# Kernel tuning notes

Measured on AMD Instinct MI355X. Metric: run time of the kernel, lower is better.

The kernel has to match this reference:

```python
import jax, jax.numpy as jnp
import numpy as np

H, V, S = 1024, 50257, 2048

def setup_inputs() -> dict:
    key = jax.random.key(0)
    ks = jax.random.split(key, 13)
    s = 0.02
    return {
        "last_output_word": jax.random.randint(ks[0], (1,), 0, V),
        "last_hidden": jax.random.normal(ks[1], (1, 1, H), dtype=jnp.float32),
        "encoder_outputs": jax.random.normal(ks[2], (S, 1, H), dtype=jnp.float32),
        "embedding": jax.random.normal(ks[3], (V, H), dtype=jnp.float32) * s,
        "attn_W": jax.random.normal(ks[4], (H, 2 * H), dtype=jnp.float32) * s,
        "attn_b": jnp.zeros((H,), dtype=jnp.float32),
        "other": jax.random.normal(ks[5], (1, H), dtype=jnp.float32) * s,
        "W_ih": jax.random.normal(ks[6], (3 * H, 2 * H), dtype=jnp.float32) * s,
        "W_hh": jax.random.normal(ks[7], (3 * H, H), dtype=jnp.float32) * s,
        "b_ih": jnp.zeros((3 * H,), dtype=jnp.float32),
        "b_hh": jnp.zeros((3 * H,), dtype=jnp.float32),
        "out_W": jax.random.normal(ks[8], (V, 2 * H), dtype=jnp.float32) * s,
        "out_b": jnp.zeros((V,), dtype=jnp.float32),
    }

def reference(last_output_word, last_hidden, encoder_outputs, embedding,
              attn_W, attn_b, other, W_ih, W_hh, b_ih, b_hh, out_W, out_b):
    h = last_hidden[-1, 0]                      # [H] top-layer hidden
    enc = encoder_outputs[:, 0, :]              # [S, H]
    # -- concat attention (vectorized over seq_len; no tanh, matches source) --
    cat = jnp.concatenate([jnp.broadcast_to(h[None, :], enc.shape), enc], axis=-1)  # [S, 2H]
    energy = cat @ attn_W.T + attn_b            # [S, H]
    scores = energy @ other[0]                  # [S]
    attn = jax.nn.softmax(scores)               # [S]
    context = attn @ enc                        # [H]
    # -- embedding (dropout = identity in eval) --
    emb = embedding[last_output_word[0]]        # [H]
    # -- single GRU step (torch gate order: r, z, n) --
    x = jnp.concatenate([emb, context])         # [2H]
    gx = W_ih @ x + b_ih                        # [3H]
    gh = W_hh @ h + b_hh                        # [3H]
    r = jax.nn.sigmoid(gx[:H] + gh[:H])
    z = jax.nn.sigmoid(gx[H:2 * H] + gh[H:2 * H])
    n = jnp.tanh(gx[2 * H:] + r * gh[2 * H:])
    h_new = (1.0 - z) * n + z * h               # [H]
    # -- output projection + log-softmax --
    logits = out_W @ jnp.concatenate([h_new, context]) + out_b   # [V]
    log_probs = jax.nn.log_softmax(logits)[None, :]              # [1, V]
    hidden = h_new[None, None, :]                                # [1, 1, H]
    attn_weights = attn[None, None, :]                           # [1, 1, S]
    return (log_probs, hidden, attn_weights)
```

## Files before the change

kernel.cpp:

```cpp
#include <hip/hip_runtime.h>
#include <math.h>

#define HD 1024
#define VD 50257
#define SD 2048


__device__ __forceinline__ float wred(float x) {
#pragma unroll
    for (int o = 32; o; o >>= 1) x += __shfl_down(x, o, 64);
    return x;
}

__global__ __launch_bounds__(256) void k_prep(
        const float* __restrict__ attn_W, const float* __restrict__ other,
        const float* __restrict__ W_hh, const float* __restrict__ h,
        const float* __restrict__ b_hh,
        const float* __restrict__ W_ih, const float* __restrict__ b_ih,
        const float* __restrict__ embedding, const int* __restrict__ word,
        float* __restrict__ ws) {
    float* u2 = ws;
    float* gA = ws + 4096;
    float* gh = ws + 7168;
    const int b = blockIdx.x, t = threadIdx.x;
    if (b < 64) {
        const int ktile = b & 3, jc = b >> 2;
        const int k = ktile * 256 + t;
        const float* Wcol = attn_W + 1024 + k;
        const int j0 = jc * 64;
        float acc = 0.f;
#pragma unroll 4
        for (int j = 0; j < 64; ++j)
            acc += other[j0 + j] * Wcol[(size_t)(j0 + j) * 2048];
        atomicAdd(&u2[k], acc);
    } else if (b < 64 + 768) {
        const int row = (b - 64) * 4 + (t >> 6);
        const int lane = t & 63;
        const float4* p = (const float4*)(W_hh + (size_t)row * 1024);
        const float4* q = (const float4*)h;
        float acc = 0.f;
#pragma unroll
        for (int i = lane; i < 256; i += 64) {
            float4 a = p[i], c = q[i];
            acc += a.x * c.x + a.y * c.y + a.z * c.z + a.w * c.w;
        }
        acc = wred(acc);
        if (lane == 0) gh[row] = acc + b_hh[row];
    } else {
        const int row = (b - 832) * 4 + (t >> 6);
        const int lane = t & 63;
        const float* emb = embedding + (size_t)word[0] * 1024;
        const float4* p = (const float4*)(W_ih + (size_t)row * 2048);
        const float4* q = (const float4*)emb;
        float acc = 0.f;
#pragma unroll
        for (int i = lane; i < 256; i += 64) {
            float4 a = p[i], c = q[i];
            acc += a.x * c.x + a.y * c.y + a.z * c.z + a.w * c.w;
        }
        acc = wred(acc);
        if (lane == 0) gA[row] = acc + b_ih[row];
    }
}

__global__ __launch_bounds__(256) void k_scores(
        const float* __restrict__ enc, const float* __restrict__ ws,
        float* __restrict__ scores) {
    const int row = blockIdx.x * 4 + (threadIdx.x >> 6);
    const int lane = threadIdx.x & 63;
    const float4* p = (const float4*)(enc + (size_t)row * 1024);
    const float4* q = (const float4*)ws;
    float acc = 0.f;
#pragma unroll
    for (int i = lane; i < 256; i += 64) {
        float4 a = p[i], c = q[i];
        acc += a.x * c.x + a.y * c.y + a.z * c.z + a.w * c.w;
    }
    acc = wred(acc);
    if (lane == 0) scores[row] = acc;
}

__global__ __launch_bounds__(256) void k_softmax(
        const float* __restrict__ scores, float* __restrict__ dout) {
    __shared__ float sm[SD];
    __shared__ float wr[8];
    __shared__ float bc;
    const int t = threadIdx.x, lane = t & 63, wave = t >> 6;
    float lm = -INFINITY;
    for (int i = t; i < SD; i += 256) {
        float x = scores[i];
        sm[i] = x;
        lm = fmaxf(lm, x);
    }
#pragma unroll
    for (int o = 32; o; o >>= 1) lm = fmaxf(lm, __shfl_down(lm, o, 64));
    if (lane == 0) wr[wave] = lm;
    __syncthreads();
    if (t == 0) bc = fmaxf(fmaxf(wr[0], wr[1]), fmaxf(wr[2], wr[3]));
    __syncthreads();
    const float M = bc;
    float ls = 0.f;
    for (int i = t; i < SD; i += 256) ls += __expf(sm[i] - M);
#pragma unroll
    for (int o = 32; o; o >>= 1) ls += __shfl_down(ls, o, 64);
    if (lane == 0) wr[4 + wave] = ls;
    __syncthreads();
    if (t == 0) bc = wr[4] + wr[5] + wr[6] + wr[7];
    __syncthreads();
    const float inv = 1.f / bc;
    for (int i = t; i < SD; i += 256) dout[VD + HD + i] = __expf(sm[i] - M) * inv;
}

__global__ __launch_bounds__(256) void k_context(
        const float* __restrict__ enc, const float* __restrict__ dout,
        float* __restrict__ context) {
    const int b = blockIdx.x;
    const int ct = b & 3, rc = b >> 2;
    const int j = ct * 256 + threadIdx.x;
    const float* attn = dout + VD + HD;
    const int r0 = rc * 128;
    float acc = 0.f;
    for (int r = 0; r < 128; ++r)
        acc += attn[r0 + r] * enc[(size_t)(r0 + r) * 1024 + j];
    atomicAdd(&context[j], acc);
}

__global__ __launch_bounds__(256) void k_gru(
        const float* __restrict__ W_ih, const float* __restrict__ h,
        float* __restrict__ ws, float* __restrict__ dout) {
    float* context = ws + 1024;
    float* gA = ws + 4096;
    float* gh = ws + 7168;
    float* y = ws + 10240;
    const int i = blockIdx.x * 4 + (threadIdx.x >> 6);
    const int lane = threadIdx.x & 63;
    const float4* q = (const float4*)context;
    float d[3];
#pragma unroll
    for (int g = 0; g < 3; ++g) {
        const float4* p = (const float4*)(W_ih + (size_t)(g * 1024 + i) * 2048 + 1024);
        float a = 0.f;
#pragma unroll
        for (int k = lane; k < 256; k += 64) {
            float4 x = p[k], c = q[k];
            a += x.x * c.x + x.y * c.y + x.z * c.z + x.w * c.w;
        }
        d[g] = wred(a);
    }
    if (lane == 0) {
        const float r = 1.f / (1.f + __expf(-(gA[i] + d[0] + gh[i])));
        const float z = 1.f / (1.f + __expf(-(gA[1024 + i] + d[1] + gh[1024 + i])));
        const float n = tanhf(gA[2048 + i] + d[2] + r * gh[2048 + i]);
        const float hn = (1.f - z) * n + z * h[i];
        dout[VD + i] = hn;
        y[i] = hn;
        y[1024 + i] = context[i];
    }
}

__global__ __launch_bounds__(256) void k_logits(
        const float* __restrict__ out_W, const float* __restrict__ out_b,
        const float* __restrict__ ws, float* __restrict__ dout) {
    __shared__ float4 sy[512];
    const float4* y4 = (const float4*)(ws + 10240);
    const int t = threadIdx.x;
    sy[t] = y4[t];
    sy[t + 256] = y4[t + 256];
    __syncthreads();
    const int row = blockIdx.x * 4 + (t >> 6);
    if (row >= VD) return;
    const int lane = t & 63;
    const float4* p = (const float4*)(out_W + (size_t)row * 2048);
    float acc = 0.f;
#pragma unroll
    for (int i = lane; i < 512; i += 64) {
        float4 a = p[i];
        float4 b = sy[i];
        acc += a.x * b.x + a.y * b.y + a.z * b.z + a.w * b.w;
    }
    acc = wred(acc);
    if (lane == 0) dout[row] = acc + out_b[row];
}

__global__ __launch_bounds__(256) void k_lse1(
        const float* __restrict__ dout, float* __restrict__ part) {
    __shared__ float wm[4], wsum[4];
    const int t = threadIdx.x, b = blockIdx.x;
    const int lane = t & 63, wave = t >> 6;
    float m = -INFINITY, s = 0.f;
    for (int v = b * 256 + t; v < VD; v += 64 * 256) {
        float x = dout[v];
        float M = fmaxf(m, x);
        s = s * __expf(m - M) + __expf(x - M);
        m = M;
    }
#pragma unroll
    for (int o = 32; o; o >>= 1) {
        float m2 = __shfl_down(m, o, 64), s2 = __shfl_down(s, o, 64);
        float M = fmaxf(m, m2);
        s = s * __expf(m - M) + s2 * __expf(m2 - M);
        m = M;
    }
    if (lane == 0) { wm[wave] = m; wsum[wave] = s; }
    __syncthreads();
    if (t == 0) {
        float M = wm[0], Ss = wsum[0];
#pragma unroll
        for (int w = 1; w < 4; ++w) {
            float M2 = fmaxf(M, wm[w]);
            Ss = Ss * __expf(M - M2) + wsum[w] * __expf(wm[w] - M2);
            M = M2;
        }
        part[2 * b] = M;
        part[2 * b + 1] = Ss;
    }
}

__global__ __launch_bounds__(256) void k_finish(
        float* __restrict__ dout, const float* __restrict__ part) {
    float m = part[0], s = part[1];
#pragma unroll 8
    for (int i = 1; i < 64; ++i) {
        float m2 = part[2 * i], s2 = part[2 * i + 1];
        float M = fmaxf(m, m2);
        s = s * __expf(m - M) + s2 * __expf(m2 - M);
        m = M;
    }
    const float lse = m + logf(s);
    for (int v = blockIdx.x * 256 + threadIdx.x; v < VD; v += gridDim.x * 256)
        dout[v] -= lse;
}

extern "C" void kernel_launch(void* const* d_in, const int* in_sizes, int n_in,
                              void* d_out, int out_size, void* d_ws, size_t ws_size,
                              hipStream_t stream) {
    const int* word = (const int*)d_in[0];
    const float* h = (const float*)d_in[1];
    const float* enc = (const float*)d_in[2];
    const float* embedding = (const float*)d_in[3];
    const float* attn_W = (const float*)d_in[4];
    const float* other = (const float*)d_in[6];
    const float* W_ih = (const float*)d_in[7];
    const float* W_hh = (const float*)d_in[8];
    const float* b_ih = (const float*)d_in[9];
    const float* b_hh = (const float*)d_in[10];
    const float* out_W = (const float*)d_in[11];
    const float* out_b = (const float*)d_in[12];
    float* out = (float*)d_out;
    float* ws = (float*)d_ws;

    hipMemsetAsync(ws, 0, 2048 * sizeof(float), stream);

    k_prep<<<1600, 256, 0, stream>>>(attn_W, other, W_hh, h, b_hh, W_ih, b_ih,
                                     embedding, word, ws);
    k_scores<<<512, 256, 0, stream>>>(enc, ws, ws + 2048);
    k_softmax<<<1, 256, 0, stream>>>(ws + 2048, out);
    k_context<<<64, 256, 0, stream>>>(enc, out, ws + 1024);
    k_gru<<<256, 256, 0, stream>>>(W_ih, h, ws, out);
    k_logits<<<(VD + 3) / 4, 256, 0, stream>>>(out_W, out_b, ws, out);
    k_lse1<<<64, 256, 0, stream>>>(out, ws + 12288);
    k_finish<<<128, 256, 0, stream>>>(out, ws + 12288);
}
```

Measured before the change: 690.8 us.

## Split output projection to overlap context half with GRU and fuse LSE partials

The output projection is split into a context half and an h_new half. The context half runs in the same launch as a fused GRU kernel (input, context and hidden matvecs together), so it no longer waits for the GRU result. Softmax is fused into the context kernel, with each block recomputing it, and the context reduction is spread over more blocks. The h_new-half kernel writes per-block max and sum-of-exp partials, and a final kernel reduces them and subtracts the log-sum-exp. This cuts launches and serialization, at the cost of redundant softmax work and a large partial-reduction repeated in every block of the last kernel.

```diff
diff --git a/kernel.cpp b/kernel.cpp
--- a/kernel.cpp
+++ b/kernel.cpp
@@ -4,6 +4,7 @@
 #define HD 1024
 #define VD 50257
 #define SD 2048
+#define NVB 12565
 
 
 __device__ __forceinline__ float wred(float x) {
@@ -12,55 +13,19 @@
     return x;
 }
 
-__global__ __launch_bounds__(256) void k_prep(
+__global__ __launch_bounds__(256) void k_u2(
         const float* __restrict__ attn_W, const float* __restrict__ other,
-        const float* __restrict__ W_hh, const float* __restrict__ h,
-        const float* __restrict__ b_hh,
-        const float* __restrict__ W_ih, const float* __restrict__ b_ih,
-        const float* __restrict__ embedding, const int* __restrict__ word,
         float* __restrict__ ws) {
-    float* u2 = ws;
-    float* gA = ws + 4096;
-    float* gh = ws + 7168;
     const int b = blockIdx.x, t = threadIdx.x;
-    if (b < 64) {
-        const int ktile = b & 3, jc = b >> 2;
-        const int k = ktile * 256 + t;
-        const float* Wcol = attn_W + 1024 + k;
-        const int j0 = jc * 64;
-        float acc = 0.f;
-#pragma unroll 4
-        for (int j = 0; j < 64; ++j)
-            acc += other[j0 + j] * Wcol[(size_t)(j0 + j) * 2048];
-        atomicAdd(&u2[k], acc);
-    } else if (b < 64 + 768) {
-        const int row = (b - 64) * 4 + (t >> 6);
-        const int lane = t & 63;
-        const float4* p = (const float4*)(W_hh + (size_t)row * 1024);
-        const float4* q = (const float4*)h;
-        float acc = 0.f;
-#pragma unroll
-        for (int i = lane; i < 256; i += 64) {
-            float4 a = p[i], c = q[i];
-            acc += a.x * c.x + a.y * c.y + a.z * c.z + a.w * c.w;
-        }
-        acc = wred(acc);
-        if (lane == 0) gh[row] = acc + b_hh[row];
-    } else {
-        const int row = (b - 832) * 4 + (t >> 6);
-        const int lane = t & 63;
-        const float* emb = embedding + (size_t)word[0] * 1024;
-        const float4* p = (const float4*)(W_ih + (size_t)row * 2048);
-        const float4* q = (const float4*)emb;
-        float acc = 0.f;
-#pragma unroll
-        for (int i = lane; i < 256; i += 64) {
-            float4 a = p[i], c = q[i];
-            acc += a.x * c.x + a.y * c.y + a.z * c.z + a.w * c.w;
-        }
-        acc = wred(acc);
-        if (lane == 0) gA[row] = acc + b_ih[row];
-    }
+    const int kt = b & 3, jc = b >> 2;
+    const int k = kt * 256 + t;
+    const float* Wcol = attn_W + HD + k;
+    const int j0 = jc * 16;
+    float acc = 0.f;
+#pragma unroll
+    for (int j = 0; j < 16; ++j)
+        acc += other[j0 + j] * Wcol[(size_t)(j0 + j) * (2 * HD)];
+    atomicAdd(&ws[k], acc);
 }
 
 __global__ __launch_bounds__(256) void k_scores(
@@ -68,7 +33,7 @@
         float* __restrict__ scores) {
     const int row = blockIdx.x * 4 + (threadIdx.x >> 6);
     const int lane = threadIdx.x & 63;
-    const float4* p = (const float4*)(enc + (size_t)row * 1024);
+    const float4* p = (const float4*)(enc + (size_t)row * HD);
     const float4* q = (const float4*)ws;
     float acc = 0.f;
 #pragma unroll
@@ -80,8 +45,9 @@
     if (lane == 0) scores[row] = acc;
 }
 
-__global__ __launch_bounds__(256) void k_softmax(
-        const float* __restrict__ scores, float* __restrict__ dout) {
+__global__ __launch_bounds__(256) void k_ctx(
+        const float* __restrict__ enc, const float* __restrict__ scores,
+        float* __restrict__ context, float* __restrict__ dout) {
     __shared__ float sm[SD];
     __shared__ float wr[8];
     __shared__ float bc;
@@ -108,90 +74,124 @@
     if (t == 0) bc = wr[4] + wr[5] + wr[6] + wr[7];
     __syncthreads();
     const float inv = 1.f / bc;
-    for (int i = t; i < SD; i += 256) dout[VD + HD + i] = __expf(sm[i] - M) * inv;
-}
-
-__global__ __launch_bounds__(256) void k_context(
-        const float* __restrict__ enc, const float* __restrict__ dout,
-        float* __restrict__ context) {
-    const int b = blockIdx.x;
-    const int ct = b & 3, rc = b >> 2;
-    const int j = ct * 256 + threadIdx.x;
-    const float* attn = dout + VD + HD;
-    const int r0 = rc * 128;
+    for (int i = t; i < SD; i += 256) sm[i] = __expf(sm[i] - M) * inv;
+    __syncthreads();
+    if (blockIdx.x == 0)
+        for (int i = t; i < SD; i += 256) dout[VD + HD + i] = sm[i];
+    const int rc = blockIdx.x >> 2, ct = blockIdx.x & 3;
+    const int j = ct * 256 + t;
+    const int r0 = rc * 64;
     float acc = 0.f;
-    for (int r = 0; r < 128; ++r)
-        acc += attn[r0 + r] * enc[(size_t)(r0 + r) * 1024 + j];
+#pragma unroll 4
+    for (int r = 0; r < 64; ++r)
+        acc += sm[r0 + r] * enc[(size_t)(r0 + r) * HD + j];
     atomicAdd(&context[j], acc);
 }
 
-__global__ __launch_bounds__(256) void k_gru(
-        const float* __restrict__ W_ih, const float* __restrict__ h,
+__global__ __launch_bounds__(256) void k_big(
+        const float* __restrict__ out_W, const float* __restrict__ W_ih,
+        const float* __restrict__ W_hh, const float* __restrict__ b_ih,
+        const float* __restrict__ b_hh, const float* __restrict__ embedding,
+        const int* __restrict__ word, const float* __restrict__ h,
         float* __restrict__ ws, float* __restrict__ dout) {
-    float* context = ws + 1024;
-    float* gA = ws + 4096;
-    float* gh = ws + 7168;
-    float* y = ws + 10240;
-    const int i = blockIdx.x * 4 + (threadIdx.x >> 6);
-    const int lane = threadIdx.x & 63;
-    const float4* q = (const float4*)context;
-    float d[3];
-#pragma unroll
-    for (int g = 0; g < 3; ++g) {
-        const float4* p = (const float4*)(W_ih + (size_t)(g * 1024 + i) * 2048 + 1024);
-        float a = 0.f;
-#pragma unroll
-        for (int k = lane; k < 256; k += 64) {
-            float4 x = p[k], c = q[k];
-            a += x.x * c.x + x.y * c.y + x.z * c.z + x.w * c.w;
-        }
-        d[g] = wred(a);
-    }
-    if (lane == 0) {
-        const float r = 1.f / (1.f + __expf(-(gA[i] + d[0] + gh[i])));
-        const float z = 1.f / (1.f + __expf(-(gA[1024 + i] + d[1] + gh[1024 + i])));
-        const float n = tanhf(gA[2048 + i] + d[2] + r * gh[2048 + i]);
-        const float hn = (1.f - z) * n + z * h[i];
-        dout[VD + i] = hn;
-        y[i] = hn;
-        y[1024 + i] = context[i];
-    }
-}
-
-__global__ __launch_bounds__(256) void k_logits(
+    __shared__ float4 sv[256];
+    const int t = threadIdx.x, lane = t & 63, wave = t >> 6;
+    const float* ctx = ws + 1024;
+    if (blockIdx.x < 256) {
+        const int i = blockIdx.x * 4 + wave;
+        const float4* e4 = (const float4*)(embedding + (size_t)word[0] * HD);
+        const float4* h4 = (const float4*)h;
+        const float4* c4 = (const float4*)ctx;
+        float ga[3], gx[3], gh[3];
+#pragma unroll
+        for (int g = 0; g < 3; ++g) {
+            const int row = g * HD + i;
+            const float4* pa = (const float4*)(W_ih + (size_t)row * 2 * HD);
+            const float4* px = pa + 256;
+            const float4* ph = (const float4*)(W_hh + (size_t)row * HD);
+            float a = 0.f, x = 0.f, hh = 0.f;
+#pragma unroll
+            for (int k = lane; k < 256; k += 64) {
+                float4 w1 = pa[k], w2 = px[k], w3 = ph[k];
+                float4 v1 = e4[k], v2 = c4[k], v3 = h4[k];
+                a += w1.x * v1.x + w1.y * v1.y + w1.z * v1.z + w1.w * v1.w;
+                x += w2.x * v2.x + w2.y * v2.y + w2.z * v2.z + w2.w * v2.w;
+                hh += w3.x * v3.x + w3.y * v3.y + w3.z * v3.z + w3.w * v3.w;
+            }
+            ga[g] = wred(a); gx[g] = wred(x); gh[g] = wred(hh);
+        }
+        if (lane == 0) {
+            const float r = 1.f / (1.f + __expf(-(ga[0] + gx[0] + b_ih[i] + gh[0] + b_hh[i])));
+            const float z = 1.f / (1.f + __expf(-(ga[1] + gx[1] + b_ih[HD + i] + gh[1] + b_hh[HD + i])));
+            const float n = tanhf(ga[2] + gx[2] + b_ih[2 * HD + i] + r * (gh[2] + b_hh[2 * HD + i]));
+            const float hn = (1.f - z) * n + z * h[i];
+            dout[VD + i] = hn;
+            ws[4096 + i] = hn;
+        }
+    } else {
+        sv[t] = ((const float4*)ctx)[t];
+        __syncthreads();
+        const int row = (blockIdx.x - 256) * 4 + wave;
+        if (row >= VD) return;
+        const float4* p = (const float4*)(out_W + (size_t)row * 2 * HD + HD);
+        float acc = 0.f;
+#pragma unroll
+        for (int i = lane; i < 256; i += 64) {
+            float4 a = p[i], c = sv[i];
+            acc += a.x * c.x + a.y * c.y + a.z * c.z + a.w * c.w;
+        }
+        acc = wred(acc);
+        if (lane == 0) ws[8192 + row] = acc;
+    }
+}
+
+__global__ __launch_bounds__(256) void k_fin(
         const float* __restrict__ out_W, const float* __restrict__ out_b,
-        const float* __restrict__ ws, float* __restrict__ dout) {
-    __shared__ float4 sy[512];
-    const float4* y4 = (const float4*)(ws + 10240);
-    const int t = threadIdx.x;
-    sy[t] = y4[t];
-    sy[t + 256] = y4[t + 256];
-    __syncthreads();
-    const int row = blockIdx.x * 4 + (t >> 6);
-    if (row >= VD) return;
-    const int lane = t & 63;
-    const float4* p = (const float4*)(out_W + (size_t)row * 2048);
-    float acc = 0.f;
-#pragma unroll
-    for (int i = lane; i < 512; i += 64) {
-        float4 a = p[i];
-        float4 b = sy[i];
-        acc += a.x * b.x + a.y * b.y + a.z * b.z + a.w * b.w;
-    }
-    acc = wred(acc);
-    if (lane == 0) dout[row] = acc + out_b[row];
-}
-
-__global__ __launch_bounds__(256) void k_lse1(
-        const float* __restrict__ dout, float* __restrict__ part) {
-    __shared__ float wm[4], wsum[4];
-    const int t = threadIdx.x, b = blockIdx.x;
-    const int lane = t & 63, wave = t >> 6;
+        float* __restrict__ ws, float* __restrict__ dout) {
+    __shared__ float4 sh[256];
+    __shared__ float lgt[4];
+    const int t = threadIdx.x, lane = t & 63, wave = t >> 6;
+    sh[t] = ((const float4*)(ws + 4096))[t];
+    __syncthreads();
+    const int row = blockIdx.x * 4 + wave;
+    float logit = -INFINITY;
+    if (row < VD) {
+        const float4* p = (const float4*)(out_W + (size_t)row * 2 * HD);
+        float acc = 0.f;
+#pragma unroll
+        for (int i = lane; i < 256; i += 64) {
+            float4 a = p[i], c = sh[i];
+            acc += a.x * c.x + a.y * c.y + a.z * c.z + a.w * c.w;
+        }
+        acc = wred(acc);
+        if (lane == 0) {
+            logit = acc + ws[8192 + row] + out_b[row];
+            dout[row] = logit;
+        }
+    }
+    if (lane == 0) lgt[wave] = logit;
+    __syncthreads();
+    if (t == 0) {
+        const float m = fmaxf(fmaxf(lgt[0], lgt[1]), fmaxf(lgt[2], lgt[3]));
+        float s = 0.f;
+#pragma unroll
+        for (int w = 0; w < 4; ++w) s += __expf(lgt[w] - m);
+        ws[61440 + 2 * blockIdx.x] = m;
+        ws[61440 + 2 * blockIdx.x + 1] = s;
+    }
+}
+
+__global__ __launch_bounds__(256) void k_sub(
+        float* __restrict__ dout, const float* __restrict__ ws) {
+    __shared__ float wm[4], wsm[4];
+    __shared__ float lsef;
+    const int t = threadIdx.x, lane = t & 63, wave = t >> 6;
+    const float* part = ws + 61440;
     float m = -INFINITY, s = 0.f;
-    for (int v = b * 256 + t; v < VD; v += 64 * 256) {
-        float x = dout[v];
-        float M = fmaxf(m, x);
-        s = s * __expf(m - M) + __expf(x - M);
+    for (int i = t; i < NVB; i += 256) {
+        float m2 = part[2 * i], s2 = part[2 * i + 1];
+        float M = fmaxf(m, m2);
+        s = s * __expf(m - M) + s2 * __expf(m2 - M);
         m = M;
     }
 #pragma unroll
@@ -201,34 +201,21 @@
         s = s * __expf(m - M) + s2 * __expf(m2 - M);
         m = M;
     }
-    if (lane == 0) { wm[wave] = m; wsum[wave] = s; }
+    if (lane == 0) { wm[wave] = m; wsm[wave] = s; }
     __syncthreads();
     if (t == 0) {
-        float M = wm[0], Ss = wsum[0];
+        float M = wm[0], S = wsm[0];
 #pragma unroll
         for (int w = 1; w < 4; ++w) {
             float M2 = fmaxf(M, wm[w]);
-            Ss = Ss * __expf(M - M2) + wsum[w] * __expf(wm[w] - M2);
+            S = S * __expf(M - M2) + wsm[w] * __expf(wm[w] - M2);
             M = M2;
         }
-        part[2 * b] = M;
-        part[2 * b + 1] = Ss;
-    }
-}
-
-__global__ __launch_bounds__(256) void k_finish(
-        float* __restrict__ dout, const float* __restrict__ part) {
-    float m = part[0], s = part[1];
-#pragma unroll 8
-    for (int i = 1; i < 64; ++i) {
-        float m2 = part[2 * i], s2 = part[2 * i + 1];
-        float M = fmaxf(m, m2);
-        s = s * __expf(m - M) + s2 * __expf(m2 - M);
-        m = M;
-    }
-    const float lse = m + logf(s);
-    for (int v = blockIdx.x * 256 + threadIdx.x; v < VD; v += gridDim.x * 256)
-        dout[v] -= lse;
+        lsef = M + logf(S);
+    }
+    __syncthreads();
+    const int v = blockIdx.x * 256 + t;
+    if (v < VD) dout[v] -= lsef;
 }
 
 extern "C" void kernel_launch(void* const* d_in, const int* in_sizes, int n_in,
@@ -250,14 +237,11 @@
     float* ws = (float*)d_ws;
 
     hipMemsetAsync(ws, 0, 2048 * sizeof(float), stream);
-
-    k_prep<<<1600, 256, 0, stream>>>(attn_W, other, W_hh, h, b_hh, W_ih, b_ih,
-                                     embedding, word, ws);
+    k_u2<<<256, 256, 0, stream>>>(attn_W, other, ws);
     k_scores<<<512, 256, 0, stream>>>(enc, ws, ws + 2048);
-    k_softmax<<<1, 256, 0, stream>>>(ws + 2048, out);
-    k_context<<<64, 256, 0, stream>>>(enc, out, ws + 1024);
-    k_gru<<<256, 256, 0, stream>>>(W_ih, h, ws, out);
-    k_logits<<<(VD + 3) / 4, 256, 0, stream>>>(out_W, out_b, ws, out);
-    k_lse1<<<64, 256, 0, stream>>>(out, ws + 12288);
-    k_finish<<<128, 256, 0, stream>>>(out, ws + 12288);
-}
+    k_ctx<<<128, 256, 0, stream>>>(enc, ws + 2048, ws + 1024, out);
+    k_big<<<256 + NVB, 256, 0, stream>>>(out_W, W_ih, W_hh, b_ih, b_hh,
+                                         embedding, word, h, ws, out);
+    k_fin<<<NVB, 256, 0, stream>>>(out_W, out_b, ws, out);
+    k_sub<<<197, 256, 0, stream>>>(out, ws);
+}
```

Result: no change. 681.1 us (-1.4%).
